# Optimization experiments

Hardware: AMD Instinct MI355X
Metric: run time of the kernel (lower is better)

The kernel has to match this reference:

```python
import jax, jax.numpy as jnp
import numpy as np

B, L, E, DK = 16, 2048, 1024, 128
MODE = "Decoder"


def setup_inputs() -> dict:
    key = jax.random.key(0)
    ks = jax.random.split(key, 6)
    x = jax.random.normal(ks[0], (B, L, E), dtype=jnp.float32)
    context = jax.random.normal(ks[1], (B, L, E), dtype=jnp.float32)
    batch_lengths = jax.random.randint(ks[2], (B,), 1, L + 1)  # valid lengths in [1, L]
    Wq = jax.random.normal(ks[3], (E, DK), dtype=jnp.float32) * 0.02
    Wk = jax.random.normal(ks[4], (E, DK), dtype=jnp.float32) * 0.02
    Wv = jax.random.normal(ks[5], (E, DK), dtype=jnp.float32) * 0.02
    return {"x": x, "context": context, "batch_lengths": batch_lengths,
            "Wq": Wq, "Wk": Wk, "Wv": Wv, "max_len": L}


def reference(x, context, batch_lengths, Wq, Wk, Wv, max_len):
    # x, context: [B, L, E]; batch_lengths: [B] ints; weights: [E, DK]
    Lq = x.shape[1]
    dk = Wq.shape[1]
    pos = jnp.arange(Lq)
    # outputMask: zero out padded time steps, broadcast over feature dim [B, L, 1]
    len_mask = (pos[None, :] < batch_lengths[:, None]).astype(x.dtype)[:, :, None]
    Q = (context @ Wq) * len_mask
    K = (context @ Wk) * len_mask
    V = (x @ Wv) * len_mask
    # energy: [B, Lq, Lk]
    energy = jnp.einsum("bqd,bkd->bqk", Q, K)
    # attnMask: -inf on padded key positions
    key_valid = pos[None, None, :] < batch_lengths[:, None, None]  # [B,1,Lk]
    if MODE == "Decoder":
        causal = pos[None, :, None] >= pos[None, None, :]  # j <= i
        key_valid = key_valid & causal
    energy = jnp.where(key_valid, energy, -jnp.inf)
    score = jax.nn.softmax(energy / jnp.sqrt(jnp.asarray(dk, x.dtype)), axis=-1)
    return jnp.einsum("bqk,bkd->bqd", score, V)
```

## Files before the change

kernel.cpp:

```cpp
#include <hip/hip_runtime.h>

#define DEV __device__ __forceinline__

typedef __attribute__((ext_vector_type(4))) float f32x4;
typedef __attribute__((ext_vector_type(4))) unsigned short u16x4;
typedef __attribute__((ext_vector_type(8))) __bf16 bf16x8;

constexpr int NB = 16, SL = 2048, EM = 1024, DKD = 128;

DEV unsigned short f2bf(float f) {
  unsigned int u = __float_as_uint(f);
  u += 0x7FFFu + ((u >> 16) & 1u);
  return (unsigned short)(u >> 16);
}

DEV f32x4 mfma16(bf16x8 a, bf16x8 b, f32x4 c) {
  return __builtin_amdgcn_mfma_f32_16x16x32_bf16(a, b, c, 0, 0, 0);
}

DEV void dma16(const void* g, void* l) {
  __builtin_amdgcn_global_load_lds(
      (const __attribute__((address_space(1))) unsigned int*)g,
      (__attribute__((address_space(3))) unsigned int*)l, 16, 0, 0);
}

DEV bf16x8 cvt8(f32x4 a, f32x4 b) {
  bf16x8 r;
  r[0] = (__bf16)a[0]; r[1] = (__bf16)a[1]; r[2] = (__bf16)a[2]; r[3] = (__bf16)a[3];
  r[4] = (__bf16)b[0]; r[5] = (__bf16)b[1]; r[6] = (__bf16)b[2]; r[7] = (__bf16)b[3];
  return r;
}

__global__ __launch_bounds__(256) void prep_w(
    const float* __restrict__ Wq, const float* __restrict__ Wk,
    const float* __restrict__ Wv, unsigned short* __restrict__ Wt)
{
  __shared__ unsigned short T[64 * 128];
  const int tid = threadIdx.x;
  const int m = blockIdx.x >> 4, kc = blockIdx.x & 15;
  const float* W = (m == 0) ? Wq : ((m == 1) ? Wk : Wv);
  #pragma unroll
  for (int it = 0; it < 8; ++it) {
    int idx = it * 256 + tid;
    int kk = idx >> 5, n4 = (idx & 31) * 4;
    f32x4 w4 = *(const f32x4*)(W + (size_t)(kc * 64 + kk) * DKD + n4);
    *(u16x4*)&T[kk * 128 + n4] =
        u16x4{ f2bf(w4[0]), f2bf(w4[1]), f2bf(w4[2]), f2bf(w4[3]) };
  }
  __syncthreads();
  #pragma unroll
  for (int it = 0; it < 4; ++it) {
    int idx = it * 256 + tid;
    int p = idx & 7, n = idx >> 3;
    int c = p ^ (n & 7);
    unsigned short v[8];
    #pragma unroll
    for (int e = 0; e < 8; ++e) v[e] = T[(c * 8 + e) * 128 + n];
    size_t t = ((size_t)(m * 16 + kc) * 128 + n) * 8 + p;
    *(u16x4*)(Wt + t * 8)     = u16x4{v[0], v[1], v[2], v[3]};
    *(u16x4*)(Wt + t * 8 + 4) = u16x4{v[4], v[5], v[6], v[7]};
  }
}

__global__ __launch_bounds__(256, 2) void proj_qk(
    const float* __restrict__ ctx, const unsigned short* __restrict__ Wt,
    const int* __restrict__ lens, unsigned short* __restrict__ Qo,
    unsigned short* __restrict__ Kz)
{
  __shared__ unsigned short Ws[2][256 * 64];
  __shared__ float Als[64 * 64];
  const int tid = threadIdx.x;
  const int wave = tid >> 6, lane = tid & 63;
  const int quad = lane >> 4, mm = lane & 15;
  const int rb = blockIdx.x * 64;

  f32x4 acc[4][4];
  #pragma unroll
  for (int i = 0; i < 4; ++i)
    #pragma unroll
    for (int j = 0; j < 4; ++j) acc[i][j] = f32x4{0.f, 0.f, 0.f, 0.f};

  const float* asrc[4];
  #pragma unroll
  for (int i = 0; i < 4; ++i) {
    const int rl_ = wave * 16 + i * 4 + (lane >> 4);
    const int cc  = (lane & 8) | ((lane & 7) ^ (rl_ & 7));
    asrc[i] = ctx + (size_t)(rb + rl_) * EM + cc * 4;
  }
  int soff[2][2];
  #pragma unroll
  for (int ks = 0; ks < 2; ++ks) {
    soff[ks][0] = (ks * 8 + ((quad * 2)     ^ (mm & 7))) * 4;
    soff[ks][1] = (ks * 8 + ((quad * 2 + 1) ^ (mm & 7))) * 4;
  }

  #pragma unroll
  for (int i = 0; i < 4; ++i)
    dma16(asrc[i], (char*)Als + wave * 4096 + i * 1024);
  #pragma unroll
  for (int it = 0; it < 8; ++it) {
    int s = it * 256 + tid;
    int mtx = s >> 10, sl = s & 1023;
    dma16(Wt + ((size_t)mtx * 16384 + sl) * 8,
          (char*)Ws[0] + (it * 256 + wave * 64) * 16);
  }
  __asm__ volatile("s_waitcnt vmcnt(8)" ::: "memory");
  __builtin_amdgcn_s_barrier();

  #pragma unroll 1
  for (int kc = 0; kc < 16; ++kc) {
    bf16x8 af[4][2];
    #pragma unroll
    for (int rt = 0; rt < 4; ++rt) {
      const float* rbase = Als + (rt * 16 + mm) * 64;
      #pragma unroll
      for (int ks = 0; ks < 2; ++ks) {
        f32x4 a0 = *(const f32x4*)(rbase + soff[ks][0]);
        f32x4 a1 = *(const f32x4*)(rbase + soff[ks][1]);
        af[rt][ks] = cvt8(a0, a1);
      }
    }
    __asm__ volatile("s_waitcnt vmcnt(0)" ::: "memory");
    __builtin_amdgcn_s_barrier();
    {
      const int kn = (kc + 1 < 16) ? (kc + 1) : 15;
      #pragma unroll
      for (int i = 0; i < 4; ++i)
        dma16(asrc[i] + kn * 64, (char*)Als + wave * 4096 + i * 1024);
      #pragma unroll
      for (int it = 0; it < 8; ++it) {
        int s = it * 256 + tid;
        int mtx = s >> 10, sl = s & 1023;
        dma16(Wt + ((size_t)mtx * 16384 + (size_t)kn * 1024 + sl) * 8,
              (char*)Ws[(kc + 1) & 1] + (it * 256 + wave * 64) * 16);
      }
    }
    {
      const unsigned short* wb = Ws[kc & 1];
      #pragma unroll
      for (int lo = 0; lo < 4; ++lo) {
        const int nrow = (wave * 4 + lo) * 16 + mm;
        #pragma unroll
        for (int ks = 0; ks < 2; ++ks) {
          const int pp = (ks * 4 + quad) ^ (mm & 7);
          bf16x8 bf = *(const bf16x8*)(wb + nrow * 64 + pp * 8);
          #pragma unroll
          for (int rt = 0; rt < 4; ++rt)
            acc[rt][lo] = mfma16(af[rt][ks], bf, acc[rt][lo]);
        }
      }
    }
    __asm__ volatile("s_waitcnt vmcnt(8)" ::: "memory");
    __builtin_amdgcn_s_barrier();
  }
  __asm__ volatile("s_waitcnt vmcnt(0)" ::: "memory");

  const int len = lens[blockIdx.x >> 5];
  const float SCALE = 1.4426950408889634f * 0.08838834764831845f;
  #pragma unroll
  for (int rt = 0; rt < 4; ++rt)
    #pragma unroll
    for (int lo = 0; lo < 4; ++lo) {
      const int ctg = wave * 4 + lo;
      #pragma unroll
      for (int reg = 0; reg < 4; ++reg) {
        const int row = rb + rt * 16 + quad * 4 + reg;
        const int j = row & (SL - 1);
        const float val = acc[rt][lo][reg];
        if (ctg < 8) {
          const int d = ctg * 16 + mm;
          Qo[(size_t)row * DKD + d] = f2bf(val * ((j < len) ? SCALE : 0.f));
        } else {
          const int d = (ctg - 8) * 16 + mm;
          Kz[(size_t)row * DKD + (((d >> 3) ^ (j & 15)) * 8) + (d & 7)] = f2bf(val);
        }
      }
    }
}

__global__ __launch_bounds__(256, 2) void proj_v(
    const float* __restrict__ x, const unsigned short* __restrict__ Wt,
    unsigned short* __restrict__ Vz)
{
  __shared__ unsigned short Ws[2][128 * 64];
  __shared__ float Als[64 * 64];
  const int tid = threadIdx.x;
  const int wave = tid >> 6, lane = tid & 63;
  const int quad = lane >> 4, mm = lane & 15;
  const int rb = blockIdx.x * 64;

  f32x4 acc[4][2];
  #pragma unroll
  for (int i = 0; i < 4; ++i) { acc[i][0] = f32x4{0.f,0.f,0.f,0.f}; acc[i][1] = f32x4{0.f,0.f,0.f,0.f}; }

  const float* asrc[4];
  #pragma unroll
  for (int i = 0; i < 4; ++i) {
    const int rl_ = wave * 16 + i * 4 + (lane >> 4);
    const int cc  = (lane & 8) | ((lane & 7) ^ (rl_ & 7));
    asrc[i] = x + (size_t)(rb + rl_) * EM + cc * 4;
  }
  int soff[2][2];
  #pragma unroll
  for (int ks = 0; ks < 2; ++ks) {
    soff[ks][0] = (ks * 8 + ((quad * 2)     ^ (mm & 7))) * 4;
    soff[ks][1] = (ks * 8 + ((quad * 2 + 1) ^ (mm & 7))) * 4;
  }

  #pragma unroll
  for (int i = 0; i < 4; ++i)
    dma16(asrc[i], (char*)Als + wave * 4096 + i * 1024);
  #pragma unroll
  for (int it = 0; it < 4; ++it) {
    int s = it * 256 + tid;
    dma16(Wt + ((size_t)2 * 16384 + s) * 8,
          (char*)Ws[0] + (it * 256 + wave * 64) * 16);
  }
  __asm__ volatile("s_waitcnt vmcnt(4)" ::: "memory");
  __builtin_amdgcn_s_barrier();

  #pragma unroll 1
  for (int kc = 0; kc < 16; ++kc) {
    bf16x8 af[4][2];
    #pragma unroll
    for (int rt = 0; rt < 4; ++rt) {
      const float* rbase = Als + (rt * 16 + mm) * 64;
      #pragma unroll
      for (int ks = 0; ks < 2; ++ks) {
        f32x4 a0 = *(const f32x4*)(rbase + soff[ks][0]);
        f32x4 a1 = *(const f32x4*)(rbase + soff[ks][1]);
        af[rt][ks] = cvt8(a0, a1);
      }
    }
    __asm__ volatile("s_waitcnt vmcnt(0)" ::: "memory");
    __builtin_amdgcn_s_barrier();
    {
      const int kn = (kc + 1 < 16) ? (kc + 1) : 15;
      #pragma unroll
      for (int i = 0; i < 4; ++i)
        dma16(asrc[i] + kn * 64, (char*)Als + wave * 4096 + i * 1024);
      #pragma unroll
      for (int it = 0; it < 4; ++it) {
        int s = it * 256 + tid;
        dma16(Wt + ((size_t)2 * 16384 + (size_t)kn * 1024 + s) * 8,
              (char*)Ws[(kc + 1) & 1] + (it * 256 + wave * 64) * 16);
      }
    }
    {
      const unsigned short* wb = Ws[kc & 1];
      #pragma unroll
      for (int lo = 0; lo < 2; ++lo) {
        const int nrow = (wave * 2 + lo) * 16 + mm;
        #pragma unroll
        for (int ks = 0; ks < 2; ++ks) {
          const int pp = (ks * 4 + quad) ^ (mm & 7);
          bf16x8 bf = *(const bf16x8*)(wb + nrow * 64 + pp * 8);
          #pragma unroll
          for (int rt = 0; rt < 4; ++rt)
            acc[rt][lo] = mfma16(af[rt][ks], bf, acc[rt][lo]);
        }
      }
    }
    __asm__ volatile("s_waitcnt vmcnt(4)" ::: "memory");
    __builtin_amdgcn_s_barrier();
  }
  __asm__ volatile("s_waitcnt vmcnt(0)" ::: "memory");

  #pragma unroll
  for (int rt = 0; rt < 4; ++rt)
    #pragma unroll
    for (int lo = 0; lo < 2; ++lo) {
      const int d = (wave * 2 + lo) * 16 + mm;
      const int row0 = rb + rt * 16 + quad * 4;
      const int b = row0 >> 11, j0 = row0 & (SL - 1);
      u16x4 pk = u16x4{ f2bf(acc[rt][lo][0]), f2bf(acc[rt][lo][1]),
                        f2bf(acc[rt][lo][2]), f2bf(acc[rt][lo][3]) };
      size_t off = (size_t)b * DKD * SL + (size_t)d * SL + (j0 & ~63)
                 + ((((j0 >> 3) & 7) ^ (d & 7)) * 8) + (j0 & 7);
      *(u16x4*)(Vz + off) = pk;
    }
}

__global__ __launch_bounds__(256, 2) void attn(
    const unsigned short* __restrict__ Qw, const unsigned short* __restrict__ Kz,
    const unsigned short* __restrict__ Vz, const int* __restrict__ lens,
    float* __restrict__ out)
{
  __shared__ unsigned short Ks[2][64 * 128];
  __shared__ unsigned short Vs[2][128 * 64];
  __shared__ unsigned short Ps[4][16 * 72];
  __shared__ float mv[128];
  const int tid = threadIdx.x;
  const int wave = tid >> 6, lane = tid & 63;
  const int quad = lane >> 4, mm = lane & 15;
  const int b = blockIdx.y;
  const int qb = ((int)gridDim.x - 1 - (int)blockIdx.x) * 64;
  const int len = lens[b];

  if (qb >= len) {
    const int half = tid >> 7, d = tid & 127, d7 = d & 7;
    const unsigned short* vbase = Vz + (size_t)b * DKD * SL + (size_t)d * SL;
    float sum = 0.f;
    for (int j0 = half * 64; j0 < len; j0 += 128) {
      #pragma unroll
      for (int cc = 0; cc < 8; ++cc) {
        const int jstart = j0 + cc * 8;
        if (jstart >= len) break;
        const unsigned short* p = vbase + j0 + ((cc ^ d7) * 8);
        if (jstart + 8 <= len) {
          bf16x8 v = *(const bf16x8*)p;
          sum += (float)v[0] + (float)v[1] + (float)v[2] + (float)v[3]
               + (float)v[4] + (float)v[5] + (float)v[6] + (float)v[7];
        } else {
          for (int r = 0; r < 8; ++r)
            if (jstart + r < len) sum += (float)*(const __bf16*)(p + r);
        }
      }
    }
    if (half == 0) mv[d] = sum;
    __syncthreads();
    if (half == 1) mv[d] += sum;
    __syncthreads();
    const float val = mv[d] / (float)len;
    #pragma unroll 1
    for (int it = 0; it < 32; ++it) {
      const int row = qb + half + it * 2;
      out[((size_t)b * SL + row) * DKD + d] = val;
    }
    return;
  }

  const int kend = min(qb + 64, len);
  const int nblk = (kend + 63) >> 6;
  const int irow0 = qb + wave * 16 + quad * 4;

  bf16x8 aQ[4];
  {
    const unsigned short* qbase =
        Qw + (size_t)(b * SL + qb + wave * 16 + mm) * DKD + quad * 8;
    #pragma unroll
    for (int cc = 0; cc < 4; ++cc) aQ[cc] = *(const bf16x8*)(qbase + cc * 32);
  }
  float mr[4], lr[4];
  #pragma unroll
  for (int r = 0; r < 4; ++r) { mr[r] = -__builtin_inff(); lr[r] = 0.f; }
  f32x4 acc[8];
  #pragma unroll
  for (int i = 0; i < 8; ++i) acc[i] = f32x4{0.f,0.f,0.f,0.f};

  #pragma unroll
  for (int it = 0; it < 4; ++it) {
    int s = it * 256 + tid;
    dma16(Kz + (size_t)(b * SL) * DKD + (size_t)s * 8,
          (char*)Ks[0] + (it * 256 + wave * 64) * 16);
  }
  #pragma unroll
  for (int it = 0; it < 4; ++it) {
    int s = it * 256 + tid;
    int d = s >> 3, p = s & 7;
    dma16(Vz + (size_t)b * DKD * SL + (size_t)d * SL + p * 8,
          (char*)Vs[0] + (it * 256 + wave * 64) * 16);
  }

  #pragma unroll 1
  for (int blk = 0; blk < nblk; ++blk) {
    const int kb = blk * 64;
    __syncthreads();
    if (blk + 1 < nblk) {
      const int kb1 = kb + 64;
      const int nb = (blk + 1) & 1;
      #pragma unroll
      for (int it = 0; it < 4; ++it) {
        int s = it * 256 + tid;
        dma16(Kz + (size_t)(b * SL + kb1) * DKD + (size_t)s * 8,
              (char*)Ks[nb] + (it * 256 + wave * 64) * 16);
      }
      #pragma unroll
      for (int it = 0; it < 4; ++it) {
        int s = it * 256 + tid;
        int d = s >> 3, p = s & 7;
        dma16(Vz + (size_t)b * DKD * SL + (size_t)d * SL + kb1 + p * 8,
              (char*)Vs[nb] + (it * 256 + wave * 64) * 16);
      }
    }
    const unsigned short* kbuf = Ks[blk & 1];
    const unsigned short* vbuf = Vs[blk & 1];

    f32x4 s4[4];
    #pragma unroll
    for (int nt = 0; nt < 4; ++nt) {
      f32x4 c = f32x4{0.f,0.f,0.f,0.f};
      const int j = nt * 16 + mm;
      #pragma unroll
      for (int cc = 0; cc < 4; ++cc) {
        const int pp = (cc * 4 + quad) ^ mm;
        bf16x8 kf = *(const bf16x8*)(kbuf + j * 128 + pp * 8);
        c = mfma16(aQ[cc], kf, c);
      }
      s4[nt] = c;
    }

    float alpha[4];
    #pragma unroll
    for (int reg = 0; reg < 4; ++reg) {
      const int jl = min(irow0 + reg + 1, len);
      float v0 = (kb + mm      < jl) ? s4[0][reg] : -__builtin_inff();
      float v1 = (kb + 16 + mm < jl) ? s4[1][reg] : -__builtin_inff();
      float v2 = (kb + 32 + mm < jl) ? s4[2][reg] : -__builtin_inff();
      float v3 = (kb + 48 + mm < jl) ? s4[3][reg] : -__builtin_inff();
      float mx = fmaxf(fmaxf(v0, v1), fmaxf(v2, v3));
      #pragma unroll
      for (int xm = 1; xm < 16; xm <<= 1) mx = fmaxf(mx, __shfl_xor(mx, xm));
      const float mn = fmaxf(mr[reg], mx);
      alpha[reg] = __builtin_amdgcn_exp2f(mr[reg] - mn);
      const float p0 = __builtin_amdgcn_exp2f(v0 - mn);
      const float p1 = __builtin_amdgcn_exp2f(v1 - mn);
      const float p2 = __builtin_amdgcn_exp2f(v2 - mn);
      const float p3 = __builtin_amdgcn_exp2f(v3 - mn);
      float sm = (p0 + p1) + (p2 + p3);
      #pragma unroll
      for (int xm = 1; xm < 16; xm <<= 1) sm += __shfl_xor(sm, xm);
      lr[reg] = lr[reg] * alpha[reg] + sm;
      mr[reg] = mn;
      const int prow = quad * 4 + reg;
      Ps[wave][prow * 72 + mm]      = f2bf(p0);
      Ps[wave][prow * 72 + 16 + mm] = f2bf(p1);
      Ps[wave][prow * 72 + 32 + mm] = f2bf(p2);
      Ps[wave][prow * 72 + 48 + mm] = f2bf(p3);
    }
    #pragma unroll
    for (int nt = 0; nt < 8; ++nt) {
      f32x4 a = acc[nt];
      a[0] *= alpha[0]; a[1] *= alpha[1]; a[2] *= alpha[2]; a[3] *= alpha[3];
      acc[nt] = a;
    }
    __asm__ volatile("s_waitcnt lgkmcnt(0)" ::: "memory");
    bf16x8 aP[2];
    #pragma unroll
    for (int ks = 0; ks < 2; ++ks)
      aP[ks] = *(const bf16x8*)(&Ps[wave][mm * 72 + ks * 32 + quad * 8]);
    #pragma unroll
    for (int ks = 0; ks < 2; ++ks)
      #pragma unroll
      for (int nt = 0; nt < 8; ++nt) {
        const int pp = (ks * 4 + quad) ^ (mm & 7);
        bf16x8 vf = *(const bf16x8*)(vbuf + (nt * 16 + mm) * 64 + pp * 8);
        acc[nt] = mfma16(aP[ks], vf, acc[nt]);
      }
  }

  #pragma unroll
  for (int reg = 0; reg < 4; ++reg) {
    const float rl = 1.0f / lr[reg];
    const size_t base = ((size_t)b * SL + irow0 + reg) * DKD + mm;
    #pragma unroll
    for (int nt = 0; nt < 8; ++nt)
      out[base + nt * 16] = acc[nt][reg] * rl;
  }
}

extern "C" void kernel_launch(void* const* d_in, const int* in_sizes, int n_in,
                              void* d_out, int out_size, void* d_ws, size_t ws_size,
                              hipStream_t stream) {
  const float* x    = (const float*)d_in[0];
  const float* ctx  = (const float*)d_in[1];
  const int*   lens = (const int*)d_in[2];
  const float* Wq   = (const float*)d_in[3];
  const float* Wk   = (const float*)d_in[4];
  const float* Wv   = (const float*)d_in[5];
  float* out = (float*)d_out;

  const size_t QKV = (size_t)NB * SL * DKD * sizeof(unsigned short);
  const size_t WTSZ = (size_t)3 * 16 * 128 * 8 * 8 * sizeof(unsigned short);
  if (ws_size < 3 * QKV + WTSZ) return;
  unsigned short* Qws = (unsigned short*)d_ws;
  unsigned short* Kzs = (unsigned short*)((char*)d_ws + QKV);
  unsigned short* Vzs = (unsigned short*)((char*)d_ws + 2 * QKV);
  unsigned short* Wt  = (unsigned short*)((char*)d_ws + 3 * QKV);

  prep_w <<<dim3(48), 256, 0, stream>>>(Wq, Wk, Wv, Wt);
  proj_qk<<<dim3(NB * SL / 64), 256, 0, stream>>>(ctx, Wt, lens, Qws, Kzs);
  proj_v <<<dim3(NB * SL / 64), 256, 0, stream>>>(x, Wt, Vzs);
  attn   <<<dim3(SL / 64, NB), 256, 0, stream>>>(Qws, Kzs, Vzs, lens, out);
}
```

Before: 377.3 us.

## Skip padded row blocks in projections and load weights directly to registers

Projection kernels now return early for 64-row blocks lying entirely beyond the sequence's valid length, avoiding reads of padded input rows. Weight tiles are loaded straight from global memory into registers instead of being staged through LDS. The freed LDS double-buffers the fp32 activation tiles with a two-ahead prefetch. Risks: uninitialized K/V workspace rows for padded blocks (relying on attention masking), and more global weight traffic per block.

```diff
diff --git a/kernel.cpp b/kernel.cpp
--- a/kernel.cpp
+++ b/kernel.cpp
@@ -30,6 +30,8 @@
   r[4] = (__bf16)b[0]; r[5] = (__bf16)b[1]; r[6] = (__bf16)b[2]; r[7] = (__bf16)b[3];
   return r;
 }
+
+#define SBAR() __builtin_amdgcn_sched_barrier(0)
 
 __global__ __launch_bounds__(256) void prep_w(
     const float* __restrict__ Wq, const float* __restrict__ Wk,
@@ -67,12 +69,13 @@
     const int* __restrict__ lens, unsigned short* __restrict__ Qo,
     unsigned short* __restrict__ Kz)
 {
-  __shared__ unsigned short Ws[2][256 * 64];
-  __shared__ float Als[64 * 64];
+  __shared__ float Als[2][64 * 64];
   const int tid = threadIdx.x;
   const int wave = tid >> 6, lane = tid & 63;
   const int quad = lane >> 4, mm = lane & 15;
   const int rb = blockIdx.x * 64;
+  const int len = lens[blockIdx.x >> 5];
+  if ((rb & (SL - 1)) >= len) return;
 
   f32x4 acc[4][4];
   #pragma unroll
@@ -93,26 +96,39 @@
     soff[ks][0] = (ks * 8 + ((quad * 2)     ^ (mm & 7))) * 4;
     soff[ks][1] = (ks * 8 + ((quad * 2 + 1) ^ (mm & 7))) * 4;
   }
+  const unsigned short* bbase[4][2];
+  #pragma unroll
+  for (int lo = 0; lo < 4; ++lo)
+    #pragma unroll
+    for (int ks = 0; ks < 2; ++ks) {
+      const int nrow = (wave * 4 + lo) * 16 + mm;
+      const int pp = (ks * 4 + quad) ^ (mm & 7);
+      const int cs = nrow * 8 + pp;
+      bbase[lo][ks] = Wt + ((size_t)(cs >> 10) * 16384 + (cs & 1023)) * 8;
+    }
 
   #pragma unroll
   for (int i = 0; i < 4; ++i)
-    dma16(asrc[i], (char*)Als + wave * 4096 + i * 1024);
-  #pragma unroll
-  for (int it = 0; it < 8; ++it) {
-    int s = it * 256 + tid;
-    int mtx = s >> 10, sl = s & 1023;
-    dma16(Wt + ((size_t)mtx * 16384 + sl) * 8,
-          (char*)Ws[0] + (it * 256 + wave * 64) * 16);
-  }
-  __asm__ volatile("s_waitcnt vmcnt(8)" ::: "memory");
+    dma16(asrc[i],      (char*)Als[0] + wave * 4096 + i * 1024);
+  #pragma unroll
+  for (int i = 0; i < 4; ++i)
+    dma16(asrc[i] + 64, (char*)Als[1] + wave * 4096 + i * 1024);
+  __asm__ volatile("s_waitcnt vmcnt(4)" ::: "memory");
   __builtin_amdgcn_s_barrier();
 
   #pragma unroll 1
   for (int kc = 0; kc < 16; ++kc) {
+    SBAR();
+    bf16x8 bfr[4][2];
+    #pragma unroll
+    for (int lo = 0; lo < 4; ++lo)
+      #pragma unroll
+      for (int ks = 0; ks < 2; ++ks)
+        bfr[lo][ks] = *(const bf16x8*)(bbase[lo][ks] + (size_t)kc * 8192);
     bf16x8 af[4][2];
     #pragma unroll
     for (int rt = 0; rt < 4; ++rt) {
-      const float* rbase = Als + (rt * 16 + mm) * 64;
+      const float* rbase = Als[kc & 1] + (rt * 16 + mm) * 64;
       #pragma unroll
       for (int ks = 0; ks < 2; ++ks) {
         f32x4 a0 = *(const f32x4*)(rbase + soff[ks][0]);
@@ -120,42 +136,26 @@
         af[rt][ks] = cvt8(a0, a1);
       }
     }
-    __asm__ volatile("s_waitcnt vmcnt(0)" ::: "memory");
+    __asm__ volatile("s_waitcnt lgkmcnt(0)" ::: "memory");
+    SBAR();
     __builtin_amdgcn_s_barrier();
     {
-      const int kn = (kc + 1 < 16) ? (kc + 1) : 15;
+      const int kn = (kc + 2 < 16) ? (kc + 2) : 15;
       #pragma unroll
       for (int i = 0; i < 4; ++i)
-        dma16(asrc[i] + kn * 64, (char*)Als + wave * 4096 + i * 1024);
-      #pragma unroll
-      for (int it = 0; it < 8; ++it) {
-        int s = it * 256 + tid;
-        int mtx = s >> 10, sl = s & 1023;
-        dma16(Wt + ((size_t)mtx * 16384 + (size_t)kn * 1024 + sl) * 8,
-              (char*)Ws[(kc + 1) & 1] + (it * 256 + wave * 64) * 16);
-      }
-    }
-    {
-      const unsigned short* wb = Ws[kc & 1];
-      #pragma unroll
-      for (int lo = 0; lo < 4; ++lo) {
-        const int nrow = (wave * 4 + lo) * 16 + mm;
+        dma16(asrc[i] + kn * 64, (char*)Als[kc & 1] + wave * 4096 + i * 1024);
+    }
+    #pragma unroll
+    for (int lo = 0; lo < 4; ++lo)
+      #pragma unroll
+      for (int ks = 0; ks < 2; ++ks)
         #pragma unroll
-        for (int ks = 0; ks < 2; ++ks) {
-          const int pp = (ks * 4 + quad) ^ (mm & 7);
-          bf16x8 bf = *(const bf16x8*)(wb + nrow * 64 + pp * 8);
-          #pragma unroll
-          for (int rt = 0; rt < 4; ++rt)
-            acc[rt][lo] = mfma16(af[rt][ks], bf, acc[rt][lo]);
-        }
-      }
-    }
-    __asm__ volatile("s_waitcnt vmcnt(8)" ::: "memory");
+        for (int rt = 0; rt < 4; ++rt)
+          acc[rt][lo] = mfma16(af[rt][ks], bfr[lo][ks], acc[rt][lo]);
     __builtin_amdgcn_s_barrier();
   }
   __asm__ volatile("s_waitcnt vmcnt(0)" ::: "memory");
 
-  const int len = lens[blockIdx.x >> 5];
   const float SCALE = 1.4426950408889634f * 0.08838834764831845f;
   #pragma unroll
   for (int rt = 0; rt < 4; ++rt)
@@ -180,14 +180,15 @@
 
 __global__ __launch_bounds__(256, 2) void proj_v(
     const float* __restrict__ x, const unsigned short* __restrict__ Wt,
-    unsigned short* __restrict__ Vz)
+    const int* __restrict__ lens, unsigned short* __restrict__ Vz)
 {
-  __shared__ unsigned short Ws[2][128 * 64];
-  __shared__ float Als[64 * 64];
+  __shared__ float Als[2][64 * 64];
   const int tid = threadIdx.x;
   const int wave = tid >> 6, lane = tid & 63;
   const int quad = lane >> 4, mm = lane & 15;
   const int rb = blockIdx.x * 64;
+  const int len = lens[blockIdx.x >> 5];
+  if ((rb & (SL - 1)) >= len) return;
 
   f32x4 acc[4][2];
   #pragma unroll
@@ -206,25 +207,39 @@
     soff[ks][0] = (ks * 8 + ((quad * 2)     ^ (mm & 7))) * 4;
     soff[ks][1] = (ks * 8 + ((quad * 2 + 1) ^ (mm & 7))) * 4;
   }
+  const unsigned short* bbase[2][2];
+  #pragma unroll
+  for (int lo = 0; lo < 2; ++lo)
+    #pragma unroll
+    for (int ks = 0; ks < 2; ++ks) {
+      const int nrow = (wave * 2 + lo) * 16 + mm;
+      const int pp = (ks * 4 + quad) ^ (mm & 7);
+      const int cs = nrow * 8 + pp;
+      bbase[lo][ks] = Wt + ((size_t)2 * 16384 + cs) * 8;
+    }
 
   #pragma unroll
   for (int i = 0; i < 4; ++i)
-    dma16(asrc[i], (char*)Als + wave * 4096 + i * 1024);
-  #pragma unroll
-  for (int it = 0; it < 4; ++it) {
-    int s = it * 256 + tid;
-    dma16(Wt + ((size_t)2 * 16384 + s) * 8,
-          (char*)Ws[0] + (it * 256 + wave * 64) * 16);
-  }
+    dma16(asrc[i],      (char*)Als[0] + wave * 4096 + i * 1024);
+  #pragma unroll
+  for (int i = 0; i < 4; ++i)
+    dma16(asrc[i] + 64, (char*)Als[1] + wave * 4096 + i * 1024);
   __asm__ volatile("s_waitcnt vmcnt(4)" ::: "memory");
   __builtin_amdgcn_s_barrier();
 
   #pragma unroll 1
   for (int kc = 0; kc < 16; ++kc) {
+    SBAR();
+    bf16x8 bfr[2][2];
+    #pragma unroll
+    for (int lo = 0; lo < 2; ++lo)
+      #pragma unroll
+      for (int ks = 0; ks < 2; ++ks)
+        bfr[lo][ks] = *(const bf16x8*)(bbase[lo][ks] + (size_t)kc * 8192);
     bf16x8 af[4][2];
     #pragma unroll
     for (int rt = 0; rt < 4; ++rt) {
-      const float* rbase = Als + (rt * 16 + mm) * 64;
+      const float* rbase = Als[kc & 1] + (rt * 16 + mm) * 64;
       #pragma unroll
       for (int ks = 0; ks < 2; ++ks) {
         f32x4 a0 = *(const f32x4*)(rbase + soff[ks][0]);
@@ -232,36 +247,22 @@
         af[rt][ks] = cvt8(a0, a1);
       }
     }
-    __asm__ volatile("s_waitcnt vmcnt(0)" ::: "memory");
+    __asm__ volatile("s_waitcnt lgkmcnt(0)" ::: "memory");
+    SBAR();
     __builtin_amdgcn_s_barrier();
     {
-      const int kn = (kc + 1 < 16) ? (kc + 1) : 15;
+      const int kn = (kc + 2 < 16) ? (kc + 2) : 15;
       #pragma unroll
       for (int i = 0; i < 4; ++i)
-        dma16(asrc[i] + kn * 64, (char*)Als + wave * 4096 + i * 1024);
-      #pragma unroll
-      for (int it = 0; it < 4; ++it) {
-        int s = it * 256 + tid;
-        dma16(Wt + ((size_t)2 * 16384 + (size_t)kn * 1024 + s) * 8,
-              (char*)Ws[(kc + 1) & 1] + (it * 256 + wave * 64) * 16);
-      }
-    }
-    {
-      const unsigned short* wb = Ws[kc & 1];
-      #pragma unroll
-      for (int lo = 0; lo < 2; ++lo) {
-        const int nrow = (wave * 2 + lo) * 16 + mm;
+        dma16(asrc[i] + kn * 64, (char*)Als[kc & 1] + wave * 4096 + i * 1024);
+    }
+    #pragma unroll
+    for (int lo = 0; lo < 2; ++lo)
+      #pragma unroll
+      for (int ks = 0; ks < 2; ++ks)
         #pragma unroll
-        for (int ks = 0; ks < 2; ++ks) {
-          const int pp = (ks * 4 + quad) ^ (mm & 7);
-          bf16x8 bf = *(const bf16x8*)(wb + nrow * 64 + pp * 8);
-          #pragma unroll
-          for (int rt = 0; rt < 4; ++rt)
-            acc[rt][lo] = mfma16(af[rt][ks], bf, acc[rt][lo]);
-        }
-      }
-    }
-    __asm__ volatile("s_waitcnt vmcnt(4)" ::: "memory");
+        for (int rt = 0; rt < 4; ++rt)
+          acc[rt][lo] = mfma16(af[rt][ks], bfr[lo][ks], acc[rt][lo]);
     __builtin_amdgcn_s_barrier();
   }
   __asm__ volatile("s_waitcnt vmcnt(0)" ::: "memory");
@@ -480,6 +481,6 @@
 
   prep_w <<<dim3(48), 256, 0, stream>>>(Wq, Wk, Wv, Wt);
   proj_qk<<<dim3(NB * SL / 64), 256, 0, stream>>>(ctx, Wt, lens, Qws, Kzs);
-  proj_v <<<dim3(NB * SL / 64), 256, 0, stream>>>(x, Wt, Vzs);
+  proj_v <<<dim3(NB * SL / 64), 256, 0, stream>>>(x, Wt, lens, Vzs);
   attn   <<<dim3(SL / 64, NB), 256, 0, stream>>>(Qws, Kzs, Vzs, lens, out);
 }
```

Result: faster. 353.4 us (-6.3%).
